# Performance work log

Measured on AMD Instinct MI355X. Metric: run time of the kernel, lower is better.

The kernel has to match this reference:

```python
import jax, jax.numpy as jnp
import numpy as np

B, N = 8, 261888
PRE_NMS_LIMIT = 6000
PROPOSAL_COUNT = 1000
SCORE_THRES = 0.5
NMS_IOU_THRES = 0.7
RPN_BBOX_STD_DEV = jnp.asarray([0.1, 0.1, 0.2, 0.2], dtype=jnp.float32)
EPS = 1e-8


def setup_inputs() -> dict:
    key = jax.random.key(0)
    k1, k2, k3, k4 = jax.random.split(key, 4)
    # class scores: softmax over (negative, positive) logits
    logits = jax.random.normal(k1, (B, N, 2), dtype=jnp.float32)
    rpn_probs = jax.nn.softmax(logits, axis=-1)
    # raw (normalized) bbox deltas; layer multiplies by RPN_BBOX_STD_DEV
    rpn_bbox = jax.random.normal(k2, (B, N, 4), dtype=jnp.float32)
    # valid normalized anchors: y1<y2, x1<x2, roughly inside [0,1]
    ctr = jax.random.uniform(k3, (B, N, 2), minval=0.05, maxval=0.95, dtype=jnp.float32)
    size = jax.random.uniform(k4, (B, N, 2), minval=0.02, maxval=0.25, dtype=jnp.float32)
    anchors = jnp.concatenate([ctr - 0.5 * size, ctr + 0.5 * size], axis=-1)  # (y1,x1,y2,x2)
    return {"rpn_probs": rpn_probs, "rpn_bbox": rpn_bbox, "anchors": anchors}


def _apply_box_deltas(boxes, deltas):
    # boxes: [..., (y1,x1,y2,x2)], deltas: [..., (dy,dx,log(dh),log(dw))]
    h = boxes[..., 2] - boxes[..., 0]
    w = boxes[..., 3] - boxes[..., 1]
    cy = boxes[..., 0] + 0.5 * h
    cx = boxes[..., 1] + 0.5 * w
    cy = cy + deltas[..., 0] * h
    cx = cx + deltas[..., 1] * w
    h = h * jnp.exp(deltas[..., 2])
    w = w * jnp.exp(deltas[..., 3])
    y1 = cy - 0.5 * h
    x1 = cx - 0.5 * w
    return jnp.stack([y1, x1, y1 + h, x1 + w], axis=-1)


def _iou_one_vs_all(box, boxes, areas):
    # box: [4], boxes: [M,4], areas: [M]
    yy1 = jnp.maximum(box[0], boxes[:, 0])
    xx1 = jnp.maximum(box[1], boxes[:, 1])
    yy2 = jnp.minimum(box[2], boxes[:, 2])
    xx2 = jnp.minimum(box[3], boxes[:, 3])
    inter = jnp.maximum(yy2 - yy1, 0.0) * jnp.maximum(xx2 - xx1, 0.0)
    area_b = (box[2] - box[0]) * (box[3] - box[1])
    return inter / (area_b + areas - inter + EPS)


def _nms_single(boxes, scores):
    # boxes: [M,4] clipped to [0,1]; scores: [M]
    areas = (boxes[:, 2] - boxes[:, 0]) * (boxes[:, 3] - boxes[:, 1])
    live = jnp.where(scores >= SCORE_THRES, scores, -1.0)

    def step(s, _):
        idx = jnp.argmax(s)
        ok = s[idx] > 0.0
        box = boxes[idx]
        iou = _iou_one_vs_all(box, boxes, areas)
        s_new = jnp.where(iou >= NMS_IOU_THRES, -1.0, s)  # self has iou=1 -> suppressed
        s_new = s_new.at[idx].set(-1.0)
        out_box = jnp.where(ok, box, jnp.zeros((4,), boxes.dtype))
        return s_new, out_box

    _, picked = jax.lax.scan(step, live, None, length=PROPOSAL_COUNT)
    return picked  # [PROPOSAL_COUNT, 4], zero-padded


def reference(rpn_probs, rpn_bbox, anchors):
    scores = rpn_probs[..., 1]                                   # [B,N]
    deltas = rpn_bbox * RPN_BBOX_STD_DEV.reshape(1, 1, 4)        # [B,N,4]
    pre_nms = min(PRE_NMS_LIMIT, scores.shape[1])
    top_scores, ix = jax.lax.top_k(scores, pre_nms)              # [B,P]
    ix4 = ix[..., None]
    deltas_top = jnp.take_along_axis(deltas, ix4, axis=1)        # [B,P,4]
    anchors_top = jnp.take_along_axis(anchors, ix4, axis=1)      # [B,P,4]
    boxes = _apply_box_deltas(anchors_top, deltas_top)
    boxes = jnp.clip(boxes, 0.0, 1.0)                            # window (0,0,1,1)
    proposals = jax.vmap(_nms_single)(boxes, top_scores)         # [B,PROPOSAL_COUNT,4]
    return proposals
```

## Files before the change

### kernel.cpp

```cpp
#include <hip/hip_runtime.h>
#include <cstdint>
#include <cstddef>

#pragma clang fp contract(off)

#define BATCH    8
#define NANCH    261888
#define PRE_NMS  6000
#define PROP     1000
#define SORTN    8192
#define NSLOT    6144
#define MROW     96
#define NW       94
#define CHUNK_W  32
#define NZCAP    128
#define NPAIR    130944
#define CBLK     64
#define CPAIR    2046
#define KCAP     1024
#define SCORE_THRES_BITS 0x3F000000u
#define EPS_F    1e-8f
#define M_D      0.6999999582767486572265625

typedef unsigned long long ull;
typedef unsigned int u32;

__global__ __launch_bounds__(256)
void hist_kernel(const float* __restrict__ rpn_probs, u32* __restrict__ ghist,
                 u32* __restrict__ done, u32* __restrict__ Tc,
                 u32* __restrict__ binbase, u32* __restrict__ cntp)
{
    __shared__ u32 h[129];
    __shared__ u32 s_old;
    const int t = threadIdx.x;
    const int b = blockIdx.y;
    if (t < 129) h[t] = 0u;
    __syncthreads();

    const float4* p4 = reinterpret_cast<const float4*>(rpn_probs + (size_t)b * NANCH * 2);
    const int p0 = blockIdx.x * CPAIR;
    for (int i = t; i < CPAIR; i += 256) {
        float4 v = p4[p0 + i];
        u32 k0 = __float_as_uint(v.y);
        u32 k1 = __float_as_uint(v.w);
        if (k0 >= 0x3F000000u) atomicAdd(&h[min((k0 >> 16) - 0x3F00u, 128u)], 1u);
        if (k1 >= 0x3F000000u) atomicAdd(&h[min((k1 >> 16) - 0x3F00u, 128u)], 1u);
    }
    __syncthreads();
    if (t < 129 && h[t]) atomicAdd(&ghist[(b << 8) + t], h[t]);

    asm volatile("s_waitcnt vmcnt(0)" ::: "memory");
    if (t == 0) s_old = atomicAdd(&done[b], 1u);
    __syncthreads();
    if (s_old == CBLK - 1) {
        if (t < 129) h[t] = atomicAdd(&ghist[(b << 8) + t], 0u);
        __syncthreads();
        if (t == 0) {
            u32* bb = binbase + b * 132;
            u32 run = 0; int binT = -1; u32 Cv = 0;
            for (int i = 128; i >= 0; --i) {
                bb[i] = run;
                run += h[i];
                if (binT < 0 && run >= PRE_NMS) { binT = i; Cv = run; }
            }
            u32 T;
            if (binT < 0)         { T = 0x3F000000u; Cv = run; }
            else if (binT == 128)   T = 0x3F800000u;
            else                    T = 0x3F000000u + ((u32)binT << 16);
            Tc[b] = T;
            cntp[b << 6] = Cv;
        }
    }
}

__global__ __launch_bounds__(256)
void compact_kernel(const float* __restrict__ rpn_probs,
                    const u32* __restrict__ Tc,
                    const u32* __restrict__ binbase,
                    u32* __restrict__ bincnt,
                    ull* __restrict__ selbuf)
{
    __shared__ ull kbuf[KCAP];
    __shared__ u32 s_n;
    __shared__ u32 s_hist[132];
    __shared__ u32 s_base[132];
    const int t    = threadIdx.x;
    const int lane = t & 63;
    const int b    = blockIdx.y;
    const u32 T = Tc[b];
    const u32* bb = binbase + b * 132;
    u32* bc = bincnt + b * 132;
    if (t == 0) s_n = 0u;
    if (t < 132) s_hist[t] = 0u;
    __syncthreads();

    const float4* p4 = reinterpret_cast<const float4*>(rpn_probs + (size_t)b * NANCH * 2);
    ull* sb = selbuf + (size_t)b * SORTN;
    const int p0 = blockIdx.x * CPAIR;

    for (int i = t; i < CPAIR; i += 256) {
        float4 v = p4[p0 + i];
        const int n0 = (p0 + i) << 1;
        #pragma unroll
        for (int e = 0; e < 2; ++e) {
            u32 k = __float_as_uint(e ? v.w : v.y);
            bool s0 = (k >= T);
            ull m = __ballot(s0 ? 1 : 0);
            if (!m) continue;
            int ldr = __ffsll(m) - 1;
            u32 base = 0;
            if (lane == ldr) base = atomicAdd(&s_n, (u32)__popcll(m));
            base = __shfl(base, ldr);
            u32 off = base + (u32)__popcll(m & ((1ull << lane) - 1ull));
            if (s0) {
                ull pk = ((ull)(~k) << 32) | (ull)(u32)(n0 + e);
                if (off < KCAP) {
                    kbuf[off] = pk;
                } else {
                    u32 bin = min((k >> 16) - 0x3F00u, 128u);
                    u32 pos = bb[bin] + atomicAdd(&bc[bin], 1u);
                    if (pos < SORTN) sb[pos] = pk;
                }
            }
        }
    }
    __syncthreads();
    const u32 nn = min(s_n, (u32)KCAP);

    for (u32 j = t; j < nn; j += 256) {
        u32 k = ~(u32)(kbuf[j] >> 32);
        atomicAdd(&s_hist[min((k >> 16) - 0x3F00u, 128u)], 1u);
    }
    __syncthreads();

    if (t < 132 && s_hist[t]) s_base[t] = atomicAdd(&bc[t], s_hist[t]);
    __syncthreads();
    if (t < 132) s_hist[t] = 0u;
    __syncthreads();

    for (u32 j = t; j < nn; j += 256) {
        ull kv = kbuf[j];
        u32 k = ~(u32)(kv >> 32);
        u32 bin = min((k >> 16) - 0x3F00u, 128u);
        u32 local = atomicAdd(&s_hist[bin], 1u);
        u32 pos = bb[bin] + s_base[bin] + local;
        if (pos < SORTN) sb[pos] = kv;
    }
}

__global__ __launch_bounds__(256)
void rank_decode_kernel(const float* __restrict__ rpn_bbox,
                        const float* __restrict__ anchors,
                        const ull* __restrict__ selbuf,
                        const u32* __restrict__ cntp,
                        const u32* __restrict__ binbase,
                        const u32* __restrict__ ghist,
                        float4* __restrict__ boxes_ws,
                        float* __restrict__ area_ws,
                        ull* __restrict__ alive_ws)
{
    const int t = threadIdx.x;
    const int b = blockIdx.y;
    const u32 C = min(cntp[b << 6], (u32)SORTN);
    const ull* sb = selbuf + (size_t)b * SORTN;

    const int i = (blockIdx.x << 8) + t;
    if (i >= (int)C) return;

    const ull mykey = sb[i];
    const u32 key = ~(u32)(mykey >> 32);
    const u32 n   = (u32)(mykey & 0xFFFFFFFFull);
    const u32 bin = min((key >> 16) - 0x3F00u, 128u);
    const u32 lo  = binbase[b * 132 + bin];
    const u32 cb  = min(ghist[(b << 8) + bin], (u32)SORTN - lo);

    const ull* base = sb + lo;
    int local = 0;
    u32 j = 0;
    for (; j + 8 <= cb; j += 8) {
        #pragma unroll
        for (int u = 0; u < 8; ++u) local += (base[j + u] < mykey) ? 1 : 0;
    }
    for (; j < cb; ++j) local += (base[j] < mykey) ? 1 : 0;
    const int rank = (int)lo + local;

    if (rank < PRE_NMS) {
        const float4* bbox4 = reinterpret_cast<const float4*>(rpn_bbox + (size_t)b * NANCH * 4);
        const float4* anc4  = reinterpret_cast<const float4*>(anchors  + (size_t)b * NANCH * 4);
        float4 a = anc4[n];
        float4 d = bbox4[n];
        float dy = d.x * 0.1f, dx = d.y * 0.1f, dh = d.z * 0.2f, dw = d.w * 0.2f;
        float h  = a.z - a.x;
        float w  = a.w - a.y;
        float cy = a.x + 0.5f * h;
        float cx = a.y + 0.5f * w;
        cy = cy + dy * h;
        cx = cx + dx * w;
        h  = h * expf(dh);
        w  = w * expf(dw);
        float y1 = cy - 0.5f * h;
        float x1 = cx - 0.5f * w;
        float y2 = y1 + h;
        float x2 = x1 + w;
        y1 = fminf(fmaxf(y1, 0.f), 1.f);
        x1 = fminf(fmaxf(x1, 0.f), 1.f);
        y2 = fminf(fmaxf(y2, 0.f), 1.f);
        x2 = fminf(fmaxf(x2, 0.f), 1.f);
        boxes_ws[(size_t)b * NSLOT + rank] = make_float4(y1, x1, y2, x2);
        area_ws[(size_t)b * NSLOT + rank]  = (y2 - y1) * (x2 - x1);
        if (key >= SCORE_THRES_BITS) {
            atomicOr(&alive_ws[(size_t)b * MROW + (rank >> 6)], 1ull << (rank & 63));
        }
    }
}

__global__ __launch_bounds__(1024)
void iou_chunk_kernel(const float4* __restrict__ boxes_ws,
                      const float* __restrict__ area_ws,
                      ull* __restrict__ mat,
                      ull* __restrict__ nzmask,
                      const u32* __restrict__ flags,
                      int kend)
{
    const int b = blockIdx.y;
    if (flags && flags[b]) return;

    __shared__ float4 sbox[NSLOT];
    __shared__ float  sarea[NSLOT];

    const int j    = blockIdx.x;
    const int t    = threadIdx.x;
    const int lane = t & 63;
    const int wv   = t >> 6;

    const int kbeg = flags ? max(j, CHUNK_W) : j;
    const int base = j << 6;
    const int nst  = (kend << 6) - base;

    const float4* bws = boxes_ws + (size_t)b * NSLOT + base;
    const float*  aws = area_ws  + (size_t)b * NSLOT + base;
    for (int i = t; i < nst; i += 1024) { sbox[i] = bws[i]; sarea[i] = aws[i]; }
    __syncthreads();

    const int r0 = base + (wv << 2);
    if (r0 >= PRE_NMS) return;

    float4 P[4];
    float  PA[4];
    #pragma unroll
    for (int qi = 0; qi < 4; ++qi) { P[qi] = sbox[(wv << 2) + qi]; PA[qi] = sarea[(wv << 2) + qi]; }

    ull* rowp = mat + ((size_t)b * PRE_NMS + r0) * MROW;
    ull acc[4] = {0ull, 0ull, 0ull, 0ull};

    for (int k = kbeg; k < kend; ++k) {
        const int ci = ((k - j) << 6) + lane;
        const float4 qb = sbox[ci];
        const float  qa = sarea[ci];
        ull m[4];
        #pragma unroll
        for (int qi = 0; qi < 4; ++qi) {
            float yy1 = fmaxf(P[qi].x, qb.x);
            float xx1 = fmaxf(P[qi].y, qb.y);
            float yy2 = fminf(P[qi].z, qb.z);
            float xx2 = fminf(P[qi].w, qb.w);
            float inter = fmaxf(yy2 - yy1, 0.f) * fmaxf(xx2 - xx1, 0.f);
            float denom = ((PA[qi] + qa) - inter) + EPS_F;
            m[qi] = __ballot(((double)inter > M_D * (double)denom) ? 1 : 0);
        }
        if (k == j) {
            #pragma unroll
            for (int qi = 0; qi < 4; ++qi) {
                int sh = (wv << 2) + qi;
                ull keep = (sh == 63) ? 0ull : ((~0ull) << (sh + 1));
                m[qi] &= keep;
            }
        }
        #pragma unroll
        for (int qi = 0; qi < 4; ++qi) acc[qi] |= m[qi];
        if (lane == 0) {
            #pragma unroll
            for (int qi = 0; qi < 4; ++qi) rowp[(size_t)qi * MROW + k] = m[qi];
        }
    }

    if (lane == 0) {
        u32 bits = 0;
        #pragma unroll
        for (int qi = 0; qi < 4; ++qi) if (acc[qi]) bits |= 1u << qi;
        if (bits) atomicOr(&nzmask[(size_t)b * NW + j], (ull)bits << (wv << 2));
    }
}

__device__ __forceinline__ ull shfl_xor64(ull x, int s)
{
    return (ull)__shfl_xor((long long)x, s, 64);
}

__device__ __forceinline__ ull readlane64(ull x, int l)
{
    u32 lo = (u32)__builtin_amdgcn_readlane((int)(u32)x, l);
    u32 hi = (u32)__builtin_amdgcn_readlane((int)(u32)(x >> 32), l);
    return ((ull)hi << 32) | (ull)lo;
}

template<bool FIRST>
__global__ __launch_bounds__(64)
__attribute__((amdgpu_waves_per_eu(1, 1)))
void nms_scan_t(const float4* __restrict__ boxes_ws,
                const ull* __restrict__ alive_ws,
                const ull* __restrict__ mat,
                const ull* __restrict__ nzmask,
                float* __restrict__ out,
                u32* __restrict__ flags)
{
    const int b = blockIdx.x;
    if (!FIRST && flags[b]) return;

    const int lane = threadIdx.x;
    const int CW = FIRST ? CHUNK_W : NW;

    __shared__ int picks[PROP];
    __shared__ u32 nzrows[NZCAP];
    __shared__ __align__(16) ull nzbuf[NZCAP * 32];

    ull aw0 = 0, aw1 = 0;
    if (lane < 48) {
        const ull* aw = alive_ws + (size_t)b * MROW + 2 * lane;
        aw0 = aw[0]; aw1 = aw[1];
    }

    const ull* mb  = mat    + (size_t)b * PRE_NMS * MROW;
    const ull* nzm = nzmask + (size_t)b * NW;

    ull nzA = 0, nzB = 0;
    if (FIRST) { if (lane < CHUNK_W) nzA = nzm[lane]; }
    else       { if (lane < 47)      { nzA = nzm[2 * lane]; nzB = nzm[2 * lane + 1]; } }

    int excl = 0, NZ = 0;
    if (FIRST) {
        int c = (int)__popcll(nzA);
        int incl = c;
        for (int s = 1; s < 32; s <<= 1) {
            int y = __shfl_up(incl, s, 64);
            if (lane >= s) incl += y;
        }
        excl = incl - c;
        NZ = __builtin_amdgcn_readlane(incl, 31);

        {
            ull m = nzA; int r = excl;
            while (m) {
                int p = __ffsll(m) - 1; m &= m - 1ull;
                if (r < NZCAP) nzrows[r] = (u32)((lane << 6) + p);
                ++r;
            }
        }
        __syncthreads();

        const int NP = min(NZ, NZCAP);
        if (NP > 0) {
            u32 ridA = nzrows[lane];
            u32 ridB = nzrows[64 + lane];
            const int ninst = (NP + 3) >> 2;
            for (int i = 0; i < ninst; ++i) {
                int slot = 4 * i + (lane >> 4);
                if (slot >= NP) slot = NP - 1;
                int sel = (slot & 63) << 2;
                int ra = __builtin_amdgcn_ds_bpermute(sel, (int)ridA);
                int rb = __builtin_amdgcn_ds_bpermute(sel, (int)ridB);
                u32 rid = (u32)((slot < 64) ? ra : rb);
                const char* src = (const char*)(mb + (size_t)rid * MROW) + ((unsigned)(lane & 15) << 4);
                __builtin_amdgcn_global_load_lds(
                    (const __attribute__((address_space(1))) void*)src,
                    (__attribute__((address_space(3))) void*)((char*)&nzbuf[0] + i * 1024),
                    16, 0, 0);
            }
        }
        asm volatile("s_waitcnt vmcnt(0)" ::: "memory");
        __builtin_amdgcn_sched_barrier(0);
    }

    int cnt = 0;
    for (int k = 0; k < CW; ++k) {
        ull nzk;
        if (FIRST) nzk = readlane64(nzA, k);
        else       nzk = readlane64((k & 1) ? nzB : nzA, k >> 1);

        const int srcw = k >> 1;
        const ull awk = (k & 1) ? aw1 : aw0;
        ull wval = readlane64(awk, srcw);

        if (wval != 0ull) {
            const int slotbase_k = FIRST ? __builtin_amdgcn_readlane(excl, k) : 0;

            ull diag_cur = 0ull;
            if (nzk != 0ull) {
                bool mynz = (nzk >> lane) & 1ull;
                if (mynz) {
                    if (FIRST) {
                        int slot = slotbase_k + (int)__popcll(nzk & ((1ull << lane) - 1ull));
                        diag_cur = (slot < NZCAP) ? nzbuf[(size_t)slot * 32 + k]
                                                  : mb[(size_t)((k << 6) + lane) * MROW + k];
                    } else {
                        diag_cur = mb[(size_t)((k << 6) + lane) * MROW + k];
                    }
                }
            }

            const bool rowAlive = (wval >> lane) & 1ull;
            ull P;
            ull conflict = (nzk == 0ull) ? 0ull
                         : __ballot((rowAlive && ((diag_cur & wval) != 0ull)) ? 1 : 0);
            if (conflict == 0ull) {
                P = wval;
            } else {
                ull T = diag_cur;
                {
                    ull y;
                    y = shfl_xor64(T, 32);
                    T = (lane & 32) ? ((T & 0xFFFFFFFF00000000ull) | ((y & 0xFFFFFFFF00000000ull) >> 32))
                                    : ((T & 0x00000000FFFFFFFFull) | ((y & 0x00000000FFFFFFFFull) << 32));
                    y = shfl_xor64(T, 16);
                    T = (lane & 16) ? ((T & 0xFFFF0000FFFF0000ull) | ((y & 0xFFFF0000FFFF0000ull) >> 16))
                                    : ((T & 0x0000FFFF0000FFFFull) | ((y & 0x0000FFFF0000FFFFull) << 16));
                    y = shfl_xor64(T, 8);
                    T = (lane & 8)  ? ((T & 0xFF00FF00FF00FF00ull) | ((y & 0xFF00FF00FF00FF00ull) >> 8))
                                    : ((T & 0x00FF00FF00FF00FFull) | ((y & 0x00FF00FF00FF00FFull) << 8));
                    y = shfl_xor64(T, 4);
                    T = (lane & 4)  ? ((T & 0xF0F0F0F0F0F0F0F0ull) | ((y & 0xF0F0F0F0F0F0F0F0ull) >> 4))
                                    : ((T & 0x0F0F0F0F0F0F0F0Full) | ((y & 0x0F0F0F0F0F0F0F0Full) << 4));
                    y = shfl_xor64(T, 2);
                    T = (lane & 2)  ? ((T & 0xCCCCCCCCCCCCCCCCull) | ((y & 0xCCCCCCCCCCCCCCCCull) >> 2))
                                    : ((T & 0x3333333333333333ull) | ((y & 0x3333333333333333ull) << 2));
                    y = shfl_xor64(T, 1);
                    T = (lane & 1)  ? ((T & 0xAAAAAAAAAAAAAAAAull) | ((y & 0xAAAAAAAAAAAAAAAAull) >> 1))
                                    : ((T & 0x5555555555555555ull) | ((y & 0x5555555555555555ull) << 1));
                }
                ull A = wval;
                P = 0ull;
                while (A) {
                    const bool inA = (A >> lane) & 1ull;
                    ull D = __ballot((inA && ((T & A) == 0ull)) ? 1 : 0);
                    P |= D;
                    ull kill = __ballot((inA && ((T & D) != 0ull)) ? 1 : 0);
                    A &= ~(D | kill);
                }
            }

            const int total = __popcll(P);
            const int room  = PROP - cnt;
            const bool lanePicked = (P >> lane) & 1ull;
            const int myrank = __popcll(P & ((1ull << lane) - 1ull));
            if (lanePicked && myrank < room) picks[cnt + myrank] = (k << 6) + lane;
            cnt = (total >= room) ? PROP : (cnt + total);

            if (cnt < PROP && nzk != 0ull) {
                ull orset = P & nzk;
                while (orset) {
                    int p = __ffsll(orset) - 1; orset &= orset - 1ull;
                    ulonglong2 v;
                    if (FIRST) {
                        int slot = slotbase_k + (int)__popcll(nzk & ((1ull << p) - 1ull));
                        if (slot < NZCAP) {
                            const ulonglong2* bv = reinterpret_cast<const ulonglong2*>(&nzbuf[(size_t)slot * 32]);
                            v = bv[lane & 15];
                        } else {
                            const ulonglong2* gv = reinterpret_cast<const ulonglong2*>(mb + (size_t)((k << 6) + p) * MROW);
                            v = gv[lane & 15];
                        }
                    } else {
                        const ulonglong2* gv = reinterpret_cast<const ulonglong2*>(mb + (size_t)((k << 6) + p) * MROW);
                        v = gv[min(lane, 47)];
                    }
                    aw0 &= ~v.x; aw1 &= ~v.y;
                }
            }
        }

        if (lane == (k >> 1)) { if (k & 1) aw1 = 0ull; else aw0 = 0ull; }
        if (cnt == PROP) break;
    }

    __syncthreads();

    if (FIRST) {
        if (cnt != PROP) return;
        if (lane == 0) flags[b] = 1u;
    }

    const float4* bws = boxes_ws + (size_t)b * NSLOT;
    float4* ob = reinterpret_cast<float4*>(out + (size_t)b * PROP * 4);
    for (int i = lane; i < PROP; i += 64) {
        float4 v = make_float4(0.f, 0.f, 0.f, 0.f);
        if (i < cnt) v = bws[picks[i]];
        ob[i] = v;
    }
}

__device__ __forceinline__ void hist_add_f(unsigned int* hist, unsigned int bin, bool valid) {
    const int lane = threadIdx.x & 63;
    ull todo = __ballot(valid ? 1 : 0);
    #pragma unroll
    for (int it = 0; it < 3; ++it) {
        if (!todo) return;
        int leader = __ffsll(todo) - 1;
        unsigned int lbin = __shfl(bin, leader);
        ull grp = __ballot((valid && (bin == lbin)) ? 1 : 0);
        if (lane == leader) atomicAdd(&hist[lbin], (unsigned int)__popcll(grp));
        todo &= ~grp;
    }
    if ((todo >> lane) & 1ull) atomicAdd(&hist[bin], 1u);
}

__global__ __launch_bounds__(1024)
void proposal_fallback(const float* __restrict__ rpn_probs,
                       const float* __restrict__ rpn_bbox,
                       const float* __restrict__ anchors,
                       float* __restrict__ out)
{
    const int b    = blockIdx.x;
    const int t    = threadIdx.x;
    const int lane = t & 63;
    const int wv   = t >> 6;

    const float2* __restrict__ probs2 = reinterpret_cast<const float2*>(rpn_probs + (size_t)b * NANCH * 2);
    const float4* __restrict__ bbox4  = reinterpret_cast<const float4*>(rpn_bbox  + (size_t)b * NANCH * 4);
    const float4* __restrict__ anc4   = reinterpret_cast<const float4*>(anchors   + (size_t)b * NANCH * 4);
    float* __restrict__ outb = out + (size_t)b * PROP * 4;

    __shared__ __align__(16) char s_big[NSLOT * 16];
    __shared__ ull          s_alive[96];
    __shared__ unsigned int s_hist[256];
    __shared__ unsigned int s_pref;
    __shared__ unsigned int s_targ;
    __shared__ unsigned int s_cnt;

    ull*    sel   = reinterpret_cast<ull*>(s_big);
    float4* boxes = reinterpret_cast<float4*>(s_big);

    const int ITER = (NANCH + 1023) >> 10;

    if (t == 0) { s_pref = 0u; s_targ = PRE_NMS; s_cnt = 0u; }

    for (int p = 0; p < 4; ++p) {
        if (t < 256) s_hist[t] = 0u;
        __syncthreads();
        const unsigned int pref  = s_pref;
        const int          shift = 8 * (3 - p);
        const unsigned int pmask = (p == 0) ? 0u : (0xFFFFFFFFu << (shift + 8));
        for (int i = 0; i < ITER; ++i) {
            int  n     = (i << 10) + t;
            bool valid = (n < NANCH);
            unsigned int key = 0u;
            if (valid) key = __float_as_uint(probs2[n].y);
            bool match = valid && ((key & pmask) == (pref & pmask));
            hist_add_f(s_hist, (key >> shift) & 0xFFu, match);
        }
        __syncthreads();
        if (t == 0) {
            unsigned int target = s_targ;
            unsigned int acc = 0u;
            int v = 255;
            for (; v >= 0; --v) {
                unsigned int h = s_hist[v];
                if (acc + h >= target) break;
                acc += h;
            }
            if (v < 0) v = 0;
            s_pref = pref | ((unsigned int)v << shift);
            s_targ = target - acc;
        }
        __syncthreads();
    }

    const unsigned int T = s_pref;
    __syncthreads();

    for (int i = 0; i < ITER; ++i) {
        int  n     = (i << 10) + t;
        bool valid = (n < NANCH);
        unsigned int key = 0u;
        if (valid) key = __float_as_uint(probs2[n].y);
        bool selp = valid && (key >= T);
        ull  m    = __ballot(selp ? 1 : 0);
        if (m) {
            int leader = __ffsll(m) - 1;
            unsigned int base = 0u;
            if (lane == leader) base = atomicAdd(&s_cnt, (unsigned int)__popcll(m));
            base = __shfl(base, leader);
            if (selp) {
                unsigned int off = base + (unsigned int)__popcll(m & ((1ull << lane) - 1ull));
                if (off < SORTN) sel[off] = ((ull)(~key) << 32) | (ull)(unsigned int)n;
            }
        }
    }
    __syncthreads();
    const unsigned int C = s_cnt;
    for (int s = (int)C + t; s < SORTN; s += 1024) sel[s] = ~0ull;
    __syncthreads();

    for (unsigned int k = 2; k <= SORTN; k <<= 1) {
        for (unsigned int j = k >> 1; j > 0; j >>= 1) {
            #pragma unroll
            for (int r = 0; r < SORTN / 1024; ++r) {
                int i = (r << 10) + t;
                int l = i ^ (int)j;
                if (l > i) {
                    ull a  = sel[i];
                    ull bq = sel[l];
                    bool up = ((i & (int)k) == 0);
                    if ((a > bq) == up) { sel[i] = bq; sel[l] = a; }
                }
            }
            __syncthreads();
        }
    }

    ull ss[6];
    #pragma unroll
    for (int e = 0; e < 6; ++e) ss[e] = sel[(e << 10) + t];
    __syncthreads();

    float4 rbox[6];
    float  rarea[6];
    #pragma unroll
    for (int e = 0; e < 6; ++e) {
        int s = (e << 10) + t;
        float4 bx = make_float4(0.f, 0.f, 0.f, 0.f);
        bool ok = false;
        if (s < PRE_NMS) {
            unsigned int key = ~(unsigned int)(ss[e] >> 32);
            unsigned int n   = (unsigned int)(ss[e] & 0xFFFFFFFFull);
            float4 a = anc4[n];
            float4 d = bbox4[n];
            float dy = d.x * 0.1f, dx = d.y * 0.1f, dh = d.z * 0.2f, dw = d.w * 0.2f;
            float h  = a.z - a.x;
            float w  = a.w - a.y;
            float cy = a.x + 0.5f * h;
            float cx = a.y + 0.5f * w;
            cy = cy + dy * h;
            cx = cx + dx * w;
            h  = h * expf(dh);
            w  = w * expf(dw);
            float y1 = cy - 0.5f * h;
            float x1 = cx - 0.5f * w;
            float y2 = y1 + h;
            float x2 = x1 + w;
            y1 = fminf(fmaxf(y1, 0.f), 1.f);
            x1 = fminf(fmaxf(x1, 0.f), 1.f);
            y2 = fminf(fmaxf(y2, 0.f), 1.f);
            x2 = fminf(fmaxf(x2, 0.f), 1.f);
            bx = make_float4(y1, x1, y2, x2);
            ok = (key >= SCORE_THRES_BITS);
        }
        rbox[e]  = bx;
        rarea[e] = (bx.z - bx.x) * (bx.w - bx.y);
        boxes[s] = bx;
        ull am = __ballot(ok ? 1 : 0);
        if (lane == 0) s_alive[wv + (e << 4)] = am;
    }

    int emitted = 0;
    for (;;) {
        __syncthreads();
        if (emitted == PROP) break;
        ull w0 = s_alive[lane];
        ull w1 = (lane < 32) ? s_alive[64 + lane] : 0ull;
        ull nz0 = __ballot(w0 != 0ull ? 1 : 0);
        ull nz1 = __ballot(w1 != 0ull ? 1 : 0);
        int pick = -1;
        if (nz0) {
            int wd = __ffsll(nz0) - 1;
            ull wvv = __shfl(w0, wd);
            pick = (wd << 6) + __ffsll(wvv) - 1;
        } else if (nz1) {
            int wd = __ffsll(nz1) - 1;
            ull wvv = __shfl(w1, wd);
            pick = ((wd + 64) << 6) + __ffsll(wvv) - 1;
        }
        if (pick < 0) break;
        __syncthreads();

        if (t < 4) outb[(emitted << 2) + t] = reinterpret_cast<const float*>(s_big)[(pick << 2) + t];

        float4 p = boxes[pick];
        float parea = (p.z - p.x) * (p.w - p.y);
        #pragma unroll
        for (int e = 0; e < 6; ++e) {
            float4 bb  = rbox[e];
            float yy1 = fmaxf(p.x, bb.x);
            float xx1 = fmaxf(p.y, bb.y);
            float yy2 = fminf(p.z, bb.z);
            float xx2 = fminf(p.w, bb.w);
            float ih  = fmaxf(yy2 - yy1, 0.f);
            float iw  = fmaxf(xx2 - xx1, 0.f);
            float inter = ih * iw;
            float denom = ((parea + rarea[e]) - inter) + EPS_F;
            bool  sup   = ((double)inter > M_D * (double)denom);
            ull m = __ballot(sup ? 1 : 0);
            int word = wv + (e << 4);
            if (word == (pick >> 6)) m |= (1ull << (pick & 63));
            if (lane == 0) s_alive[word] &= ~m;
        }
        ++emitted;
    }

    for (int i = (emitted << 2) + t; i < PROP * 4; i += 1024) outb[i] = 0.f;
}

extern "C" void kernel_launch(void* const* d_in, const int* in_sizes, int n_in,
                              void* d_out, int out_size, void* d_ws, size_t ws_size,
                              hipStream_t stream) {
    const float* rpn_probs = (const float*)d_in[0];
    const float* rpn_bbox  = (const float*)d_in[1];
    const float* anchors   = (const float*)d_in[2];
    float* out = (float*)d_out;

    const size_t BOX_OFF   = 0;
    const size_t AREA_OFF  = 786432;
    const size_t ZERO_OFF  = 983040;
    const size_t ALIVE_OFF = 983040;
    const size_t TC_OFF    = 989184;
    const size_t DONE_OFF  = 989440;
    const size_t CNT_OFF   = 989696;
    const size_t GHIST_OFF = 991744;
    const size_t FLAG_OFF  = 999936;
    const size_t BINB_OFF  = 1000448;
    const size_t BINC_OFF  = 1004672;
    const size_t NZ_OFF    = 1008896;
    const size_t MAT_OFF   = 1u << 20;
    const size_t SELB_OFF  = MAT_OFF;
    const size_t WS_NEED   = MAT_OFF + (size_t)BATCH * PRE_NMS * MROW * 8;

    if (d_ws != nullptr && ws_size >= WS_NEED) {
        char* ws = (char*)d_ws;
        float4* boxes_ws = (float4*)(ws + BOX_OFF);
        float*  area_ws  = (float*)(ws + AREA_OFF);
        ull*    alive_ws = (ull*)(ws + ALIVE_OFF);
        u32*    Tc       = (u32*)(ws + TC_OFF);
        u32*    done     = (u32*)(ws + DONE_OFF);
        u32*    cntp     = (u32*)(ws + CNT_OFF);
        u32*    ghist    = (u32*)(ws + GHIST_OFF);
        u32*    flags    = (u32*)(ws + FLAG_OFF);
        u32*    binbase  = (u32*)(ws + BINB_OFF);
        u32*    bincnt   = (u32*)(ws + BINC_OFF);
        ull*    nzmask   = (ull*)(ws + NZ_OFF);
        ull*    selbuf   = (ull*)(ws + SELB_OFF);
        ull*    mat      = (ull*)(ws + MAT_OFF);

        hipMemsetAsync(ws + ZERO_OFF, 0, MAT_OFF - ZERO_OFF, stream);
        hipLaunchKernelGGL(hist_kernel, dim3(CBLK, BATCH), dim3(256), 0, stream,
                           rpn_probs, ghist, done, Tc, binbase, cntp);
        hipLaunchKernelGGL(compact_kernel, dim3(CBLK, BATCH), dim3(256), 0, stream,
                           rpn_probs, Tc, binbase, bincnt, selbuf);
        hipLaunchKernelGGL(rank_decode_kernel, dim3(SORTN / 256, BATCH), dim3(256), 0, stream,
                           rpn_bbox, anchors, selbuf, cntp, binbase, ghist,
                           boxes_ws, area_ws, alive_ws);
        hipLaunchKernelGGL(iou_chunk_kernel, dim3(CHUNK_W, BATCH), dim3(1024), 0, stream,
                           boxes_ws, area_ws, mat, nzmask, (const u32*)nullptr, CHUNK_W);
        hipLaunchKernelGGL((nms_scan_t<true>), dim3(BATCH), dim3(64), 0, stream,
                           boxes_ws, alive_ws, mat, nzmask, out, flags);
        hipLaunchKernelGGL(iou_chunk_kernel, dim3(NW, BATCH), dim3(1024), 0, stream,
                           boxes_ws, area_ws, mat, nzmask, (const u32*)flags, NW);
        hipLaunchKernelGGL((nms_scan_t<false>), dim3(BATCH), dim3(64), 0, stream,
                           boxes_ws, alive_ws, mat, nzmask, out, flags);
    } else {
        hipLaunchKernelGGL(proposal_fallback, dim3(BATCH), dim3(1024), 0, stream,
                           rpn_probs, rpn_bbox, anchors, out);
    }
}
```

Before: 202.4 us.

## Fuse seven launches into two persistent kernels with intra-grid spin barriers

Merges the histogram, compaction and rank/decode kernels into one front kernel, and the IoU chunk and two NMS scan kernels into one back kernel. Stages are chained by device-scope atomic tickets with release/acquire fences and sleeping spin-waits instead of separate launches. This removes launch gaps and per-kernel ramp-up between short dependent stages. In exchange it relies on every block of a batch being co-resident, or the spin-waits deadlock. It also leaves the scan's non-zero-row staging and the rank stage with only 128 active threads per block.

Measured after the change: 341.5 us. 1.69x slower.

```diff
diff --git a/kernel.cpp b/kernel.cpp
--- a/kernel.cpp
+++ b/kernel.cpp
@@ -25,20 +25,44 @@
 typedef unsigned long long ull;
 typedef unsigned int u32;
 
-__global__ __launch_bounds__(256)
-void hist_kernel(const float* __restrict__ rpn_probs, u32* __restrict__ ghist,
-                 u32* __restrict__ done, u32* __restrict__ Tc,
-                 u32* __restrict__ binbase, u32* __restrict__ cntp)
+
+__device__ __forceinline__ void fence_release_agent()
 {
-    __shared__ u32 h[129];
-    __shared__ u32 s_old;
-    const int t = threadIdx.x;
-    const int b = blockIdx.y;
-    if (t < 129) h[t] = 0u;
+    __builtin_amdgcn_fence(__ATOMIC_RELEASE, "agent");
+}
+__device__ __forceinline__ void fence_acquire_agent()
+{
+    __builtin_amdgcn_fence(__ATOMIC_ACQUIRE, "agent");
+}
+
+__global__ __launch_bounds__(256, 2)
+void front_kernel(const float* __restrict__ rpn_probs,
+                  const float* __restrict__ rpn_bbox,
+                  const float* __restrict__ anchors,
+                  u32* __restrict__ ghist, u32* __restrict__ done,
+                  u32* __restrict__ Tc, u32* __restrict__ binbase,
+                  u32* __restrict__ cntp, u32* __restrict__ bincnt,
+                  ull* __restrict__ selbuf, u32* __restrict__ done2,
+                  float4* __restrict__ boxes_ws, float* __restrict__ area_ws,
+                  ull* __restrict__ alive_ws)
+{
+    const int t    = threadIdx.x;
+    const int lane = t & 63;
+    const int b    = blockIdx.y;
+    const int x    = blockIdx.x;
+
+    __shared__ u32 h[132];
+    __shared__ u32 s_old, s_T, s_n;
+    __shared__ ull kbuf[KCAP];
+    __shared__ u32 s_hist[132];
+    __shared__ u32 s_base[132];
+    __shared__ u32 s_bb[132];
+
+    if (t < 132) h[t] = 0u;
     __syncthreads();
 
     const float4* p4 = reinterpret_cast<const float4*>(rpn_probs + (size_t)b * NANCH * 2);
-    const int p0 = blockIdx.x * CPAIR;
+    const int p0 = x * CPAIR;
     for (int i = t; i < CPAIR; i += 256) {
         float4 v = p4[p0 + i];
         u32 k0 = __float_as_uint(v.y);
@@ -67,36 +91,27 @@
             if (binT < 0)         { T = 0x3F000000u; Cv = run; }
             else if (binT == 128)   T = 0x3F800000u;
             else                    T = 0x3F000000u + ((u32)binT << 16);
-            Tc[b] = T;
             cntp[b << 6] = Cv;
-        }
-    }
-}
-
-__global__ __launch_bounds__(256)
-void compact_kernel(const float* __restrict__ rpn_probs,
-                    const u32* __restrict__ Tc,
-                    const u32* __restrict__ binbase,
-                    u32* __restrict__ bincnt,
-                    ull* __restrict__ selbuf)
-{
-    __shared__ ull kbuf[KCAP];
-    __shared__ u32 s_n;
-    __shared__ u32 s_hist[132];
-    __shared__ u32 s_base[132];
-    const int t    = threadIdx.x;
-    const int lane = t & 63;
-    const int b    = blockIdx.y;
-    const u32 T = Tc[b];
-    const u32* bb = binbase + b * 132;
-    u32* bc = bincnt + b * 132;
+            fence_release_agent();
+            atomicExch(&Tc[b], T);
+        }
+    }
+
+    if (t == 0) {
+        u32 T;
+        while ((T = atomicAdd(&Tc[b], 0u)) == 0u) __builtin_amdgcn_s_sleep(8);
+        s_T = T;
+    }
+    __syncthreads();
+    fence_acquire_agent();
+    if (t < 132) s_bb[t] = binbase[b * 132 + t];
     if (t == 0) s_n = 0u;
     if (t < 132) s_hist[t] = 0u;
     __syncthreads();
-
-    const float4* p4 = reinterpret_cast<const float4*>(rpn_probs + (size_t)b * NANCH * 2);
+    const u32 T = s_T;
+
     ull* sb = selbuf + (size_t)b * SORTN;
-    const int p0 = blockIdx.x * CPAIR;
+    u32* bc = bincnt + b * 132;
 
     for (int i = t; i < CPAIR; i += 256) {
         float4 v = p4[p0 + i];
@@ -118,7 +133,7 @@
                     kbuf[off] = pk;
                 } else {
                     u32 bin = min((k >> 16) - 0x3F00u, 128u);
-                    u32 pos = bb[bin] + atomicAdd(&bc[bin], 1u);
+                    u32 pos = s_bb[bin] + atomicAdd(&bc[bin], 1u);
                     if (pos < SORTN) sb[pos] = pk;
                 }
             }
@@ -132,46 +147,37 @@
         atomicAdd(&s_hist[min((k >> 16) - 0x3F00u, 128u)], 1u);
     }
     __syncthreads();
-
     if (t < 132 && s_hist[t]) s_base[t] = atomicAdd(&bc[t], s_hist[t]);
     __syncthreads();
     if (t < 132) s_hist[t] = 0u;
     __syncthreads();
-
     for (u32 j = t; j < nn; j += 256) {
         ull kv = kbuf[j];
         u32 k = ~(u32)(kv >> 32);
         u32 bin = min((k >> 16) - 0x3F00u, 128u);
         u32 local = atomicAdd(&s_hist[bin], 1u);
-        u32 pos = bb[bin] + s_base[bin] + local;
+        u32 pos = s_bb[bin] + s_base[bin] + local;
         if (pos < SORTN) sb[pos] = kv;
     }
-}
-
-__global__ __launch_bounds__(256)
-void rank_decode_kernel(const float* __restrict__ rpn_bbox,
-                        const float* __restrict__ anchors,
-                        const ull* __restrict__ selbuf,
-                        const u32* __restrict__ cntp,
-                        const u32* __restrict__ binbase,
-                        const u32* __restrict__ ghist,
-                        float4* __restrict__ boxes_ws,
-                        float* __restrict__ area_ws,
-                        ull* __restrict__ alive_ws)
-{
-    const int t = threadIdx.x;
-    const int b = blockIdx.y;
+
+    fence_release_agent();
+    if (t == 0) atomicAdd(&done2[b], 1u);
+
+    if (t == 0) {
+        while (atomicAdd(&done2[b], 0u) < (u32)CBLK) __builtin_amdgcn_s_sleep(8);
+    }
+    __syncthreads();
+    fence_acquire_agent();
+
     const u32 C = min(cntp[b << 6], (u32)SORTN);
-    const ull* sb = selbuf + (size_t)b * SORTN;
-
-    const int i = (blockIdx.x << 8) + t;
-    if (i >= (int)C) return;
+    const int i = (x << 7) + t;
+    if (t >= 128 || i >= (int)C) return;
 
     const ull mykey = sb[i];
     const u32 key = ~(u32)(mykey >> 32);
     const u32 n   = (u32)(mykey & 0xFFFFFFFFull);
     const u32 bin = min((key >> 16) - 0x3F00u, 128u);
-    const u32 lo  = binbase[b * 132 + bin];
+    const u32 lo  = s_bb[bin];
     const u32 cb  = min(ghist[(b << 8) + bin], (u32)SORTN - lo);
 
     const ull* base = sb + lo;
@@ -190,18 +196,18 @@
         float4 a = anc4[n];
         float4 d = bbox4[n];
         float dy = d.x * 0.1f, dx = d.y * 0.1f, dh = d.z * 0.2f, dw = d.w * 0.2f;
-        float h  = a.z - a.x;
-        float w  = a.w - a.y;
-        float cy = a.x + 0.5f * h;
-        float cx = a.y + 0.5f * w;
-        cy = cy + dy * h;
-        cx = cx + dx * w;
-        h  = h * expf(dh);
-        w  = w * expf(dw);
-        float y1 = cy - 0.5f * h;
-        float x1 = cx - 0.5f * w;
-        float y2 = y1 + h;
-        float x2 = x1 + w;
+        float hh = a.z - a.x;
+        float ww = a.w - a.y;
+        float cy = a.x + 0.5f * hh;
+        float cx = a.y + 0.5f * ww;
+        cy = cy + dy * hh;
+        cx = cx + dx * ww;
+        hh = hh * expf(dh);
+        ww = ww * expf(dw);
+        float y1 = cy - 0.5f * hh;
+        float x1 = cx - 0.5f * ww;
+        float y2 = y1 + hh;
+        float x2 = x1 + ww;
         y1 = fminf(fmaxf(y1, 0.f), 1.f);
         x1 = fminf(fmaxf(x1, 0.f), 1.f);
         y2 = fminf(fmaxf(y2, 0.f), 1.f);
@@ -214,82 +220,70 @@
     }
 }
 
-__global__ __launch_bounds__(1024)
-void iou_chunk_kernel(const float4* __restrict__ boxes_ws,
-                      const float* __restrict__ area_ws,
-                      ull* __restrict__ mat,
-                      ull* __restrict__ nzmask,
-                      const u32* __restrict__ flags,
-                      int kend)
+__device__ void iou_block(const float4* __restrict__ bws_b,
+                          const float* __restrict__ aws_b,
+                          ull* __restrict__ mat_b, ull* __restrict__ nzm_b,
+                          int j, int kbeg, int kend,
+                          float4* sbox, float* sarea)
 {
-    const int b = blockIdx.y;
-    if (flags && flags[b]) return;
-
-    __shared__ float4 sbox[NSLOT];
-    __shared__ float  sarea[NSLOT];
-
-    const int j    = blockIdx.x;
     const int t    = threadIdx.x;
     const int lane = t & 63;
     const int wv   = t >> 6;
-
-    const int kbeg = flags ? max(j, CHUNK_W) : j;
     const int base = j << 6;
     const int nst  = (kend << 6) - base;
 
-    const float4* bws = boxes_ws + (size_t)b * NSLOT + base;
-    const float*  aws = area_ws  + (size_t)b * NSLOT + base;
-    for (int i = t; i < nst; i += 1024) { sbox[i] = bws[i]; sarea[i] = aws[i]; }
+    for (int i = t; i < nst; i += 1024) { sbox[i] = bws_b[base + i]; sarea[i] = aws_b[base + i]; }
     __syncthreads();
 
     const int r0 = base + (wv << 2);
-    if (r0 >= PRE_NMS) return;
-
-    float4 P[4];
-    float  PA[4];
-    #pragma unroll
-    for (int qi = 0; qi < 4; ++qi) { P[qi] = sbox[(wv << 2) + qi]; PA[qi] = sarea[(wv << 2) + qi]; }
-
-    ull* rowp = mat + ((size_t)b * PRE_NMS + r0) * MROW;
-    ull acc[4] = {0ull, 0ull, 0ull, 0ull};
-
-    for (int k = kbeg; k < kend; ++k) {
-        const int ci = ((k - j) << 6) + lane;
-        const float4 qb = sbox[ci];
-        const float  qa = sarea[ci];
-        ull m[4];
+    if (r0 < PRE_NMS) {
+        float4 P[4];
+        float  PA[4];
         #pragma unroll
-        for (int qi = 0; qi < 4; ++qi) {
-            float yy1 = fmaxf(P[qi].x, qb.x);
-            float xx1 = fmaxf(P[qi].y, qb.y);
-            float yy2 = fminf(P[qi].z, qb.z);
-            float xx2 = fminf(P[qi].w, qb.w);
-            float inter = fmaxf(yy2 - yy1, 0.f) * fmaxf(xx2 - xx1, 0.f);
-            float denom = ((PA[qi] + qa) - inter) + EPS_F;
-            m[qi] = __ballot(((double)inter > M_D * (double)denom) ? 1 : 0);
-        }
-        if (k == j) {
+        for (int qi = 0; qi < 4; ++qi) { P[qi] = sbox[(wv << 2) + qi]; PA[qi] = sarea[(wv << 2) + qi]; }
+
+        ull* rowp = mat_b + (size_t)r0 * MROW;
+        ull acc[4] = {0ull, 0ull, 0ull, 0ull};
+
+        for (int k = kbeg; k < kend; ++k) {
+            const int ci = ((k - j) << 6) + lane;
+            const float4 qb = sbox[ci];
+            const float  qa = sarea[ci];
+            ull m[4];
             #pragma unroll
             for (int qi = 0; qi < 4; ++qi) {
-                int sh = (wv << 2) + qi;
-                ull keep = (sh == 63) ? 0ull : ((~0ull) << (sh + 1));
-                m[qi] &= keep;
-            }
-        }
-        #pragma unroll
-        for (int qi = 0; qi < 4; ++qi) acc[qi] |= m[qi];
+                float yy1 = fmaxf(P[qi].x, qb.x);
+                float xx1 = fmaxf(P[qi].y, qb.y);
+                float yy2 = fminf(P[qi].z, qb.z);
+                float xx2 = fminf(P[qi].w, qb.w);
+                float inter = fmaxf(yy2 - yy1, 0.f) * fmaxf(xx2 - xx1, 0.f);
+                float denom = ((PA[qi] + qa) - inter) + EPS_F;
+                m[qi] = __ballot(((double)inter > M_D * (double)denom) ? 1 : 0);
+            }
+            if (k == j) {
+                #pragma unroll
+                for (int qi = 0; qi < 4; ++qi) {
+                    int sh = (wv << 2) + qi;
+                    ull keep = (sh == 63) ? 0ull : ((~0ull) << (sh + 1));
+                    m[qi] &= keep;
+                }
+            }
+            #pragma unroll
+            for (int qi = 0; qi < 4; ++qi) acc[qi] |= m[qi];
+            if (lane == 0) {
+                #pragma unroll
+                for (int qi = 0; qi < 4; ++qi) rowp[(size_t)qi * MROW + k] = m[qi];
+            }
+        }
+
         if (lane == 0) {
+            u32 bits = 0;
             #pragma unroll
-            for (int qi = 0; qi < 4; ++qi) rowp[(size_t)qi * MROW + k] = m[qi];
-        }
-    }
-
-    if (lane == 0) {
-        u32 bits = 0;
-        #pragma unroll
-        for (int qi = 0; qi < 4; ++qi) if (acc[qi]) bits |= 1u << qi;
-        if (bits) atomicOr(&nzmask[(size_t)b * NW + j], (ull)bits << (wv << 2));
-    }
+            for (int qi = 0; qi < 4; ++qi) if (acc[qi]) bits |= 1u << qi;
+            if (bits) atomicOr(&nzm_b[j], (ull)bits << (wv << 2));
+        }
+    }
+    __syncthreads();
 }
 
 __device__ __forceinline__ ull shfl_xor64(ull x, int s)
@@ -305,33 +299,22 @@
 }
 
 template<bool FIRST>
-__global__ __launch_bounds__(64)
-__attribute__((amdgpu_waves_per_eu(1, 1)))
-void nms_scan_t(const float4* __restrict__ boxes_ws,
-                const ull* __restrict__ alive_ws,
-                const ull* __restrict__ mat,
-                const ull* __restrict__ nzmask,
-                float* __restrict__ out,
-                u32* __restrict__ flags)
+__device__ void scan_wave(int b, int lane,
+                          const float4* __restrict__ bws_b,
+                          const ull* __restrict__ alive_ws,
+                          const ull* __restrict__ mb,
+                          const ull* __restrict__ nzm,
+                          float* __restrict__ out,
+                          u32* __restrict__ flags,
+                          int* picks, u32* nzrows, ull* nzbuf)
 {
-    const int b = blockIdx.x;
-    if (!FIRST && flags[b]) return;
-
-    const int lane = threadIdx.x;
     const int CW = FIRST ? CHUNK_W : NW;
-
-    __shared__ int picks[PROP];
-    __shared__ u32 nzrows[NZCAP];
-    __shared__ __align__(16) ull nzbuf[NZCAP * 32];
 
     ull aw0 = 0, aw1 = 0;
     if (lane < 48) {
         const ull* aw = alive_ws + (size_t)b * MROW + 2 * lane;
         aw0 = aw[0]; aw1 = aw[1];
     }
-
-    const ull* mb  = mat    + (size_t)b * PRE_NMS * MROW;
-    const ull* nzm = nzmask + (size_t)b * NW;
 
     ull nzA = 0, nzB = 0;
     if (FIRST) { if (lane < CHUNK_W) nzA = nzm[lane]; }
@@ -356,8 +339,6 @@
                 ++r;
             }
         }
-        __syncthreads();
-
         const int NP = min(NZ, NZCAP);
         if (NP > 0) {
             u32 ridA = nzrows[lane];
@@ -373,7 +354,7 @@
                 const char* src = (const char*)(mb + (size_t)rid * MROW) + ((unsigned)(lane & 15) << 4);
                 __builtin_amdgcn_global_load_lds(
                     (const __attribute__((address_space(1))) void*)src,
-                    (__attribute__((address_space(3))) void*)((char*)&nzbuf[0] + i * 1024),
+                    (__attribute__((address_space(3))) void*)((char*)nzbuf + i * 1024),
                     16, 0, 0);
             }
         }
@@ -415,35 +396,35 @@
             if (conflict == 0ull) {
                 P = wval;
             } else {
-                ull T = diag_cur;
+                ull Tt = diag_cur;
                 {
                     ull y;
-                    y = shfl_xor64(T, 32);
-                    T = (lane & 32) ? ((T & 0xFFFFFFFF00000000ull) | ((y & 0xFFFFFFFF00000000ull) >> 32))
-                                    : ((T & 0x00000000FFFFFFFFull) | ((y & 0x00000000FFFFFFFFull) << 32));
-                    y = shfl_xor64(T, 16);
-                    T = (lane & 16) ? ((T & 0xFFFF0000FFFF0000ull) | ((y & 0xFFFF0000FFFF0000ull) >> 16))
-                                    : ((T & 0x0000FFFF0000FFFFull) | ((y & 0x0000FFFF0000FFFFull) << 16));
-                    y = shfl_xor64(T, 8);
-                    T = (lane & 8)  ? ((T & 0xFF00FF00FF00FF00ull) | ((y & 0xFF00FF00FF00FF00ull) >> 8))
-                                    : ((T & 0x00FF00FF00FF00FFull) | ((y & 0x00FF00FF00FF00FFull) << 8));
-                    y = shfl_xor64(T, 4);
-                    T = (lane & 4)  ? ((T & 0xF0F0F0F0F0F0F0F0ull) | ((y & 0xF0F0F0F0F0F0F0F0ull) >> 4))
-                                    : ((T & 0x0F0F0F0F0F0F0F0Full) | ((y & 0x0F0F0F0F0F0F0F0Full) << 4));
-                    y = shfl_xor64(T, 2);
-                    T = (lane & 2)  ? ((T & 0xCCCCCCCCCCCCCCCCull) | ((y & 0xCCCCCCCCCCCCCCCCull) >> 2))
-                                    : ((T & 0x3333333333333333ull) | ((y & 0x3333333333333333ull) << 2));
-                    y = shfl_xor64(T, 1);
-                    T = (lane & 1)  ? ((T & 0xAAAAAAAAAAAAAAAAull) | ((y & 0xAAAAAAAAAAAAAAAAull) >> 1))
-                                    : ((T & 0x5555555555555555ull) | ((y & 0x5555555555555555ull) << 1));
+                    y = shfl_xor64(Tt, 32);
+                    Tt = (lane & 32) ? ((Tt & 0xFFFFFFFF00000000ull) | ((y & 0xFFFFFFFF00000000ull) >> 32))
+                                     : ((Tt & 0x00000000FFFFFFFFull) | ((y & 0x00000000FFFFFFFFull) << 32));
+                    y = shfl_xor64(Tt, 16);
+                    Tt = (lane & 16) ? ((Tt & 0xFFFF0000FFFF0000ull) | ((y & 0xFFFF0000FFFF0000ull) >> 16))
+                                     : ((Tt & 0x0000FFFF0000FFFFull) | ((y & 0x0000FFFF0000FFFFull) << 16));
+                    y = shfl_xor64(Tt, 8);
+                    Tt = (lane & 8)  ? ((Tt & 0xFF00FF00FF00FF00ull) | ((y & 0xFF00FF00FF00FF00ull) >> 8))
+                                     : ((Tt & 0x00FF00FF00FF00FFull) | ((y & 0x00FF00FF00FF00FFull) << 8));
+                    y = shfl_xor64(Tt, 4);
+                    Tt = (lane & 4)  ? ((Tt & 0xF0F0F0F0F0F0F0F0ull) | ((y & 0xF0F0F0F0F0F0F0F0ull) >> 4))
+                                     : ((Tt & 0x0F0F0F0F0F0F0F0Full) | ((y & 0x0F0F0F0F0F0F0F0Full) << 4));
+                    y = shfl_xor64(Tt, 2);
+                    Tt = (lane & 2)  ? ((Tt & 0xCCCCCCCCCCCCCCCCull) | ((y & 0xCCCCCCCCCCCCCCCCull) >> 2))
+                                     : ((Tt & 0x3333333333333333ull) | ((y & 0x3333333333333333ull) << 2));
+                    y = shfl_xor64(Tt, 1);
+                    Tt = (lane & 1)  ? ((Tt & 0xAAAAAAAAAAAAAAAAull) | ((y & 0xAAAAAAAAAAAAAAAAull) >> 1))
+                                     : ((Tt & 0x5555555555555555ull) | ((y & 0x5555555555555555ull) << 1));
                 }
                 ull A = wval;
                 P = 0ull;
                 while (A) {
                     const bool inA = (A >> lane) & 1ull;
-                    ull D = __ballot((inA && ((T & A) == 0ull)) ? 1 : 0);
+                    ull D = __ballot((inA && ((Tt & A) == 0ull)) ? 1 : 0);
                     P |= D;
-                    ull kill = __ballot((inA && ((T & D) != 0ull)) ? 1 : 0);
+                    ull kill = __ballot((inA && ((Tt & D) != 0ull)) ? 1 : 0);
                     A &= ~(D | kill);
                 }
             }
@@ -463,7 +444,7 @@
                     if (FIRST) {
                         int slot = slotbase_k + (int)__popcll(nzk & ((1ull << p) - 1ull));
                         if (slot < NZCAP) {
-                            const ulonglong2* bv = reinterpret_cast<const ulonglong2*>(&nzbuf[(size_t)slot * 32]);
+                            const ulonglong2* bv = reinterpret_cast<const ulonglong2*>(nzbuf + (size_t)slot * 32);
                             v = bv[lane & 15];
                         } else {
                             const ulonglong2* gv = reinterpret_cast<const ulonglong2*>(mb + (size_t)((k << 6) + p) * MROW);
@@ -482,19 +463,78 @@
         if (cnt == PROP) break;
     }
 
-    __syncthreads();
-
     if (FIRST) {
-        if (cnt != PROP) return;
-        if (lane == 0) flags[b] = 1u;
-    }
-
-    const float4* bws = boxes_ws + (size_t)b * NSLOT;
+        if (cnt != PROP) {
+            if (lane == 0) atomicExch(&flags[b], 2u);
+            return;
+        }
+        if (lane == 0) atomicExch(&flags[b], 1u);
+    }
+
     float4* ob = reinterpret_cast<float4*>(out + (size_t)b * PROP * 4);
     for (int i = lane; i < PROP; i += 64) {
         float4 v = make_float4(0.f, 0.f, 0.f, 0.f);
-        if (i < cnt) v = bws[picks[i]];
+        if (i < cnt) v = bws_b[picks[i]];
         ob[i] = v;
+    }
+}
+
+__global__ __launch_bounds__(1024, 4)
+void back_kernel(const float4* __restrict__ boxes_ws, const float* __restrict__ area_ws,
+                 ull* __restrict__ mat, ull* __restrict__ nzmask,
+                 const ull* __restrict__ alive_ws,
+                 u32* __restrict__ flags, u32* __restrict__ ticket3, u32* __restrict__ ticket4,
+                 float* __restrict__ out)
+{
+    const int b  = blockIdx.y;
+    const int jj = blockIdx.x;
+    const int t  = threadIdx.x;
+
+    __shared__ float4 sbox[NSLOT];
+    __shared__ __align__(16) ull nzbuf[NZCAP * 32];
+    __shared__ float  sarea[NSLOT];
+    __shared__ int    picks[PROP];
+    __shared__ u32    nzrows[NZCAP];
+    __shared__ u32    s_flag;
+
+    const float4* bws_b = boxes_ws + (size_t)b * NSLOT;
+    const float*  aws_b = area_ws  + (size_t)b * NSLOT;
+    ull* mat_b = mat    + (size_t)b * PRE_NMS * MROW;
+    ull* nzm_b = nzmask + (size_t)b * NW;
+
+    iou_block(bws_b, aws_b, mat_b, nzm_b, jj, jj, CHUNK_W, sbox, sarea);
+    fence_release_agent();
+    if (t == 0) atomicAdd(&ticket3[b], 1u);
+
+    if (jj == 0 && t < 64) {
+        if (t == 0) {
+            while (atomicAdd(&ticket3[b], 0u) < (u32)CHUNK_W) __builtin_amdgcn_s_sleep(8);
+        }
+        fence_acquire_agent();
+        scan_wave<true>(b, t, bws_b, alive_ws, mat_b, nzm_b, out, flags,
+                        picks, nzrows, nzbuf);
+    }
+
+    if (t == 0) {
+        u32 f;
+        while ((f = atomicAdd(&flags[b], 0u)) == 0u) __builtin_amdgcn_s_sleep(8);
+        s_flag = f;
+    }
+    __syncthreads();
+    if (s_flag == 1u) return;
+
+    for (int j = jj; j < NW; j += CHUNK_W)
+        iou_block(bws_b, aws_b, mat_b, nzm_b, j, max(j, CHUNK_W), NW, sbox, sarea);
+    fence_release_agent();
+    if (t == 0) atomicAdd(&ticket4[b], 1u);
+
+    if (jj == 0 && t < 64) {
+        if (t == 0) {
+            while (atomicAdd(&ticket4[b], 0u) < (u32)CHUNK_W) __builtin_amdgcn_s_sleep(8);
+        }
+        fence_acquire_agent();
+        scan_wave<false>(b, t, bws_b, alive_ws, mat_b, nzm_b, out, flags,
+                         picks, nzrows, nzbuf);
     }
 }
 
@@ -729,6 +769,9 @@
     const size_t BINB_OFF  = 1000448;
     const size_t BINC_OFF  = 1004672;
     const size_t NZ_OFF    = 1008896;
+    const size_t DONE2_OFF = 1014912;
+    const size_t TK3_OFF   = 1015424;
+    const size_t TK4_OFF   = 1015936;
     const size_t MAT_OFF   = 1u << 20;
     const size_t SELB_OFF  = MAT_OFF;
     const size_t WS_NEED   = MAT_OFF + (size_t)BATCH * PRE_NMS * MROW * 8;
@@ -746,25 +789,20 @@
         u32*    binbase  = (u32*)(ws + BINB_OFF);
         u32*    bincnt   = (u32*)(ws + BINC_OFF);
         ull*    nzmask   = (ull*)(ws + NZ_OFF);
+        u32*    done2    = (u32*)(ws + DONE2_OFF);
+        u32*    ticket3  = (u32*)(ws + TK3_OFF);
+        u32*    ticket4  = (u32*)(ws + TK4_OFF);
         ull*    selbuf   = (ull*)(ws + SELB_OFF);
         ull*    mat      = (ull*)(ws + MAT_OFF);
 
         hipMemsetAsync(ws + ZERO_OFF, 0, MAT_OFF - ZERO_OFF, stream);
-        hipLaunchKernelGGL(hist_kernel, dim3(CBLK, BATCH), dim3(256), 0, stream,
-                           rpn_probs, ghist, done, Tc, binbase, cntp);
-        hipLaunchKernelGGL(compact_kernel, dim3(CBLK, BATCH), dim3(256), 0, stream,
-                           rpn_probs, Tc, binbase, bincnt, selbuf);
-        hipLaunchKernelGGL(rank_decode_kernel, dim3(SORTN / 256, BATCH), dim3(256), 0, stream,
-                           rpn_bbox, anchors, selbuf, cntp, binbase, ghist,
+        hipLaunchKernelGGL(front_kernel, dim3(CBLK, BATCH), dim3(256), 0, stream,
+                           rpn_probs, rpn_bbox, anchors,
+                           ghist, done, Tc, binbase, cntp, bincnt, selbuf, done2,
                            boxes_ws, area_ws, alive_ws);
-        hipLaunchKernelGGL(iou_chunk_kernel, dim3(CHUNK_W, BATCH), dim3(1024), 0, stream,
-                           boxes_ws, area_ws, mat, nzmask, (const u32*)nullptr, CHUNK_W);
-        hipLaunchKernelGGL((nms_scan_t<true>), dim3(BATCH), dim3(64), 0, stream,
-                           boxes_ws, alive_ws, mat, nzmask, out, flags);
-        hipLaunchKernelGGL(iou_chunk_kernel, dim3(NW, BATCH), dim3(1024), 0, stream,
-                           boxes_ws, area_ws, mat, nzmask, (const u32*)flags, NW);
-        hipLaunchKernelGGL((nms_scan_t<false>), dim3(BATCH), dim3(64), 0, stream,
-                           boxes_ws, alive_ws, mat, nzmask, out, flags);
+        hipLaunchKernelGGL(back_kernel, dim3(CHUNK_W, BATCH), dim3(1024), 0, stream,
+                           boxes_ws, area_ws, mat, nzmask, alive_ws,
+                           flags, ticket3, ticket4, out);
     } else {
         hipLaunchKernelGGL(proposal_fallback, dim3(BATCH), dim3(1024), 0, stream,
                            rpn_probs, rpn_bbox, anchors, out);
```
